# Performance work log

Measured on AMD Instinct MI355X. Metric: run time of the kernel, lower is better.

The kernel has to match this reference:

```python
import jax, jax.numpy as jnp
import numpy as np
import math

H = 512
N2 = 32  # N // 2
L_VAL = 8192
DT_MIN, DT_MAX = 0.001, 0.1


def setup_inputs() -> dict:
    key = jax.random.key(0)
    k1, k2, k3 = jax.random.split(key, 3)
    log_dt = jax.random.uniform(k1, (H,), dtype=jnp.float32) * (
        math.log(DT_MAX) - math.log(DT_MIN)) + math.log(DT_MIN)
    B_real = jax.random.normal(k2, (H, N2), dtype=jnp.float32)
    B_imag = jax.random.normal(k3, (H, N2), dtype=jnp.float32)
    C = jnp.ones((H, N2), dtype=jnp.float32)
    Kc = jnp.ones((H, N2), dtype=jnp.float32)
    A_real = jnp.log(0.5 * jnp.ones((H, N2), dtype=jnp.float32))
    A_imag = jnp.broadcast_to(math.pi * jnp.arange(N2, dtype=jnp.float32), (H, N2))
    return {"log_dt": log_dt, "B_real": B_real, "B_imag": B_imag,
            "C": C, "Kc": Kc, "A_real": A_real, "A_imag": A_imag, "L": L_VAL}


def reference(log_dt, B_real, B_imag, C, Kc, A_real, A_imag, L):
    dt = jnp.exp(log_dt)[:, None]                      # (H, 1)
    A = -jnp.exp(A_real) - 1e-6 + 1j * A_imag          # (H, N2) complex
    denom = 1.0 - dt * A / 2 + 1e-6                    # bilinear denominator
    dtA = (1.0 + dt * A / 2) / denom                   # discretized A (H, N2)
    B = B_real + 1j * B_imag
    dtB = dt * B / denom                               # discretized B (H, N2)
    log_dtA = jnp.log(dtA)                             # complex log
    # Vandermonde in log space: (H, N2, L) complex — the big intermediate.
    V = jnp.exp(log_dtA[:, :, None] * jnp.arange(L, dtype=jnp.float32))
    Cc = C.astype(dtB.dtype) * dtB                     # (H, N2) complex
    K = 2.0 * jnp.einsum('hn,hnl->hl', Cc, V).real     # (H, L)
    return K
```

## Files before the change

### kernel.cpp

```cpp
#include <hip/hip_runtime.h>
#include <math.h>

#define HN   512
#define N2M  32
#define LVAL 8192
#define TPB  256
#define STR  136
#define STRD 68

typedef _Float16 f16x8 __attribute__((ext_vector_type(8)));
typedef float    f32x4 __attribute__((ext_vector_type(4)));

__device__ __forceinline__ void split_store(unsigned* dst_hi, unsigned* dst_lo,
                                            float x, float y) {
    const _Float16 hx = (_Float16)x, hy = (_Float16)y;
    const float lxf = x - (float)hx, lyf = y - (float)hy;
    const _Float16 lx = (_Float16)lxf, ly = (_Float16)lyf;
    const unsigned short ux = __builtin_bit_cast(unsigned short, hx);
    const unsigned short uy = __builtin_bit_cast(unsigned short, hy);
    const unsigned short vx = __builtin_bit_cast(unsigned short, lx);
    const unsigned short vy = __builtin_bit_cast(unsigned short, ly);
    *dst_hi = (unsigned)ux | ((unsigned)uy << 16);
    *dst_lo = (unsigned)vx | ((unsigned)vy << 16);
}

__global__ __launch_bounds__(TPB, 4) void s4d_mfma(
    const float* __restrict__ log_dt,
    const float* __restrict__ B_real,
    const float* __restrict__ B_imag,
    const float* __restrict__ Cmat,
    const float* __restrict__ A_real,
    const float* __restrict__ A_imag,
    float* __restrict__ out)
{
    __shared__ __align__(16) _Float16 shU[64 * STR];
    __shared__ __align__(16) _Float16 shW[64 * STR];
    __shared__ float pm[N2M][12];

    const int h  = blockIdx.y;
    const int bx = blockIdx.x;
    const int t  = threadIdx.x;

    if (t < N2M) {
        const int idx = h * N2M + t;
        const float dt  = expf(log_dt[h]);
        const float Are = -expf(A_real[idx]) - 1e-6f;
        const float Aim = A_imag[idx];
        const float hdt = 0.5f * dt;
        const float dre  = 1.0f - hdt * Are + 1e-6f;
        const float dim_ = -hdt * Aim;
        const float nre = 1.0f + hdt * Are;
        const float nim = hdt * Aim;
        const float inv = 1.0f / (dre * dre + dim_ * dim_);
        const float zr = (nre * dre + nim * dim_) * inv;
        const float zi = (nim * dre - nre * dim_) * inv;
        const float br = B_real[idx], bi = B_imag[idx];
        const float tbr = dt * ((br * dre + bi * dim_) * inv);
        const float tbi = dt * ((bi * dre - br * dim_) * inv);
        const float Cv = Cmat[idx];
        const float c2r = 2.0f * Cv * tbr;
        const float c2i = 2.0f * Cv * tbi;
        const float r2  = zr * zr + zi * zi;
        const float xl2 = 0.5f * log2f(r2);
        const float phi = atan2f(zi, zr) * 0.15915494309189535f;
        const float ph  = __uint_as_float(__float_as_uint(phi) & 0xFFFFE000u);
        const float pl  = phi - ph;
        const float e64   = __builtin_amdgcn_exp2f(64.0f * xl2);
        const float rev64 = __builtin_amdgcn_fractf(
            fmaf(64.0f, pl, __builtin_amdgcn_fractf(64.0f * ph)));
        const float z64r = e64 * __builtin_amdgcn_cosf(rev64);
        const float z64i = e64 * __builtin_amdgcn_sinf(rev64);
        pm[t][0] = xl2; pm[t][1] = ph;  pm[t][2] = pl;
        pm[t][3] = c2r; pm[t][4] = c2i;
        pm[t][5] = zr;  pm[t][6] = zi;
        pm[t][7] = z64r; pm[t][8] = z64i;
    }
    __syncthreads();

    {
        const int n  = t >> 3;
        const int j0 = (t & 7) * 8;
        const float xl2 = pm[n][0], ph = pm[n][1], pl = pm[n][2];
        const float zr  = pm[n][5], zi = pm[n][6];
        const float j0f = (float)j0;
        const float e   = __builtin_amdgcn_exp2f(j0f * xl2);
        const float rev = __builtin_amdgcn_fractf(
            fmaf(j0f, pl, __builtin_amdgcn_fractf(j0f * ph)));
        float wr = e * __builtin_amdgcn_cosf(rev);
        float wi = e * __builtin_amdgcn_sinf(rev);
        unsigned* dw = (unsigned*)shW;
#pragma unroll
        for (int jj = 0; jj < 8; ++jj) {
            const int j = j0 + jj;
            split_store(dw + j * STRD + n, dw + j * STRD + 32 + n, wr, -wi);
            const float nwr = wr * zr - wi * zi;
            wi = fmaf(wr, zi, wi * zr);
            wr = nwr;
        }
    }

    {
        const int n  = t >> 3;
        const int m0 = (t & 7) * 8;
        const float xl2 = pm[n][0], ph = pm[n][1], pl = pm[n][2];
        const float c2r = pm[n][3], c2i = pm[n][4];
        const float z64r = pm[n][7], z64i = pm[n][8];
        const float l0f = (float)((bx << 12) + (m0 << 6));
        const float e   = __builtin_amdgcn_exp2f(l0f * xl2);
        const float rev = __builtin_amdgcn_fractf(
            fmaf(l0f, pl, __builtin_amdgcn_fractf(l0f * ph)));
        const float cs_ = __builtin_amdgcn_cosf(rev);
        const float sn_ = __builtin_amdgcn_sinf(rev);
        float ur = e * fmaf(c2r, cs_, -(c2i * sn_));
        float ui = e * fmaf(c2r, sn_, c2i * cs_);
        unsigned* dw = (unsigned*)shU;
#pragma unroll
        for (int mm = 0; mm < 8; ++mm) {
            const int m = m0 + mm;
            split_store(dw + m * STRD + n, dw + m * STRD + 32 + n, ur, ui);
            const float nur = ur * z64r - ui * z64i;
            ui = fmaf(ur, z64i, ui * z64r);
            ur = nur;
        }
    }
    __syncthreads();

    const int w = t >> 6, lane = t & 63, g = lane >> 4, r = lane & 15;
    const _Float16* ua = shU + (w * 16 + r) * STR + g * 8;
    const f16x8 A0 = *(const f16x8*)(ua);
    const f16x8 A1 = *(const f16x8*)(ua + 32);
    const f16x8 A2 = *(const f16x8*)(ua + 64);
    const f16x8 A3 = *(const f16x8*)(ua + 96);
    float* outp = out + (size_t)h * LVAL + (bx << 12);
#pragma unroll
    for (int jt = 0; jt < 4; ++jt) {
        const _Float16* wb = shW + (jt * 16 + r) * STR + g * 8;
        const f16x8 B0 = *(const f16x8*)(wb);
        const f16x8 B1 = *(const f16x8*)(wb + 32);
        const f16x8 B2 = *(const f16x8*)(wb + 64);
        const f16x8 B3 = *(const f16x8*)(wb + 96);
        f32x4 acc = {0.f, 0.f, 0.f, 0.f};
        acc = __builtin_amdgcn_mfma_f32_16x16x32_f16(A0, B0, acc, 0, 0, 0);
        acc = __builtin_amdgcn_mfma_f32_16x16x32_f16(A1, B1, acc, 0, 0, 0);
        acc = __builtin_amdgcn_mfma_f32_16x16x32_f16(A2, B0, acc, 0, 0, 0);
        acc = __builtin_amdgcn_mfma_f32_16x16x32_f16(A3, B1, acc, 0, 0, 0);
        acc = __builtin_amdgcn_mfma_f32_16x16x32_f16(A0, B2, acc, 0, 0, 0);
        acc = __builtin_amdgcn_mfma_f32_16x16x32_f16(A1, B3, acc, 0, 0, 0);
        const int jcol = jt * 16 + r;
#pragma unroll
        for (int rr = 0; rr < 4; ++rr) {
            const int m_local = w * 16 + g * 4 + rr;
            outp[m_local * 64 + jcol] = acc[rr];
        }
    }
}

extern "C" void kernel_launch(void* const* d_in, const int* in_sizes, int n_in,
                              void* d_out, int out_size, void* d_ws, size_t ws_size,
                              hipStream_t stream)
{
    const float* log_dt = (const float*)d_in[0];
    const float* B_real = (const float*)d_in[1];
    const float* B_imag = (const float*)d_in[2];
    const float* Cmat   = (const float*)d_in[3];
    const float* A_real = (const float*)d_in[5];
    const float* A_imag = (const float*)d_in[6];
    float* out = (float*)d_out;

    dim3 grid(2, HN);
    s4d_mfma<<<grid, dim3(TPB), 0, stream>>>(log_dt, B_real, B_imag, Cmat,
                                             A_real, A_imag, out);
}
```

Measured before the change: 13.58 us.

## Split per-mode parameter setup into a separate precompute kernel via workspace

Moves the per-(h,n) discretization math (exp, log2, atan2, sin/cos) out of the MFMA kernel into a small setup kernel that writes 12 floats per mode to the workspace. The main kernel then loads these with float4 reads into shared memory instead of having 32 threads compute them serially while the rest of the block waits. This removes the duplicated setup across the two x-blocks per row and shortens the serial prologue. In exchange it adds a second kernel launch and a global round trip, and drops the occupancy hint from launch_bounds.

```diff
diff --git a/kernel.cpp b/kernel.cpp
--- a/kernel.cpp
+++ b/kernel.cpp
@@ -24,64 +24,74 @@
     *dst_lo = (unsigned)vx | ((unsigned)vy << 16);
 }
 
-__global__ __launch_bounds__(TPB, 4) void s4d_mfma(
+__global__ __launch_bounds__(128) void s4d_setup(
     const float* __restrict__ log_dt,
     const float* __restrict__ B_real,
     const float* __restrict__ B_imag,
     const float* __restrict__ Cmat,
     const float* __restrict__ A_real,
     const float* __restrict__ A_imag,
+    float* __restrict__ ws)
+{
+    const int i = blockIdx.x * 128 + threadIdx.x;
+    if (i >= HN * N2M) return;
+    const int h = i >> 5;
+    const float dt  = expf(log_dt[h]);
+    const float Are = -expf(A_real[i]) - 1e-6f;
+    const float Aim = A_imag[i];
+    const float hdt = 0.5f * dt;
+    const float dre  = 1.0f - hdt * Are + 1e-6f;
+    const float dim_ = -hdt * Aim;
+    const float nre = 1.0f + hdt * Are;
+    const float nim = hdt * Aim;
+    const float inv = 1.0f / (dre * dre + dim_ * dim_);
+    const float zr = (nre * dre + nim * dim_) * inv;
+    const float zi = (nim * dre - nre * dim_) * inv;
+    const float br = B_real[i], bi = B_imag[i];
+    const float tbr = dt * ((br * dre + bi * dim_) * inv);
+    const float tbi = dt * ((bi * dre - br * dim_) * inv);
+    const float Cv = Cmat[i];
+    const float c2r = 2.0f * Cv * tbr;
+    const float c2i = 2.0f * Cv * tbi;
+    const float r2  = zr * zr + zi * zi;
+    const float xl2 = 0.5f * log2f(r2);
+    const float phi = atan2f(zi, zr) * 0.15915494309189535f;
+    const float ph  = __uint_as_float(__float_as_uint(phi) & 0xFFFFE000u);
+    const float pl  = phi - ph;
+    const float e64   = __builtin_amdgcn_exp2f(64.0f * xl2);
+    const float rev64 = __builtin_amdgcn_fractf(
+        fmaf(64.0f, pl, __builtin_amdgcn_fractf(64.0f * ph)));
+    const float z64r = e64 * __builtin_amdgcn_cosf(rev64);
+    const float z64i = e64 * __builtin_amdgcn_sinf(rev64);
+    float4* w4 = (float4*)(ws + (size_t)i * 12);
+    w4[0] = make_float4(xl2, ph, pl, c2r);
+    w4[1] = make_float4(c2i, zr, zi, z64r);
+    w4[2] = make_float4(z64i, 0.0f, 0.0f, 0.0f);
+}
+
+__global__ __launch_bounds__(TPB) void s4d_mfma(
+    const float* __restrict__ ws,
     float* __restrict__ out)
 {
     __shared__ __align__(16) _Float16 shU[64 * STR];
     __shared__ __align__(16) _Float16 shW[64 * STR];
-    __shared__ float pm[N2M][12];
+    __shared__ float4 pm4[N2M * 3];
 
     const int h  = blockIdx.y;
     const int bx = blockIdx.x;
     const int t  = threadIdx.x;
 
-    if (t < N2M) {
-        const int idx = h * N2M + t;
-        const float dt  = expf(log_dt[h]);
-        const float Are = -expf(A_real[idx]) - 1e-6f;
-        const float Aim = A_imag[idx];
-        const float hdt = 0.5f * dt;
-        const float dre  = 1.0f - hdt * Are + 1e-6f;
-        const float dim_ = -hdt * Aim;
-        const float nre = 1.0f + hdt * Are;
-        const float nim = hdt * Aim;
-        const float inv = 1.0f / (dre * dre + dim_ * dim_);
-        const float zr = (nre * dre + nim * dim_) * inv;
-        const float zi = (nim * dre - nre * dim_) * inv;
-        const float br = B_real[idx], bi = B_imag[idx];
-        const float tbr = dt * ((br * dre + bi * dim_) * inv);
-        const float tbi = dt * ((bi * dre - br * dim_) * inv);
-        const float Cv = Cmat[idx];
-        const float c2r = 2.0f * Cv * tbr;
-        const float c2i = 2.0f * Cv * tbi;
-        const float r2  = zr * zr + zi * zi;
-        const float xl2 = 0.5f * log2f(r2);
-        const float phi = atan2f(zi, zr) * 0.15915494309189535f;
-        const float ph  = __uint_as_float(__float_as_uint(phi) & 0xFFFFE000u);
-        const float pl  = phi - ph;
-        const float e64   = __builtin_amdgcn_exp2f(64.0f * xl2);
-        const float rev64 = __builtin_amdgcn_fractf(
-            fmaf(64.0f, pl, __builtin_amdgcn_fractf(64.0f * ph)));
-        const float z64r = e64 * __builtin_amdgcn_cosf(rev64);
-        const float z64i = e64 * __builtin_amdgcn_sinf(rev64);
-        pm[t][0] = xl2; pm[t][1] = ph;  pm[t][2] = pl;
-        pm[t][3] = c2r; pm[t][4] = c2i;
-        pm[t][5] = zr;  pm[t][6] = zi;
-        pm[t][7] = z64r; pm[t][8] = z64i;
+    if (t < N2M * 3) {
+        pm4[t] = ((const float4*)ws)[h * (N2M * 3) + t];
     }
     __syncthreads();
+    const float* pm = (const float*)pm4;
 
     {
         const int n  = t >> 3;
         const int j0 = (t & 7) * 8;
-        const float xl2 = pm[n][0], ph = pm[n][1], pl = pm[n][2];
-        const float zr  = pm[n][5], zi = pm[n][6];
+        const float xl2 = pm[n * 12 + 0], ph = pm[n * 12 + 1], pl = pm[n * 12 + 2];
+        const float zr  = pm[n * 12 + 5], zi = pm[n * 12 + 6];
         const float j0f = (float)j0;
         const float e   = __builtin_amdgcn_exp2f(j0f * xl2);
         const float rev = __builtin_amdgcn_fractf(
@@ -102,9 +112,9 @@
     {
         const int n  = t >> 3;
         const int m0 = (t & 7) * 8;
-        const float xl2 = pm[n][0], ph = pm[n][1], pl = pm[n][2];
-        const float c2r = pm[n][3], c2i = pm[n][4];
-        const float z64r = pm[n][7], z64i = pm[n][8];
+        const float xl2 = pm[n * 12 + 0], ph = pm[n * 12 + 1], pl = pm[n * 12 + 2];
+        const float c2r = pm[n * 12 + 3], c2i = pm[n * 12 + 4];
+        const float z64r = pm[n * 12 + 7], z64i = pm[n * 12 + 8];
         const float l0f = (float)((bx << 12) + (m0 << 6));
         const float e   = __builtin_amdgcn_exp2f(l0f * xl2);
         const float rev = __builtin_amdgcn_fractf(
@@ -166,8 +176,11 @@
     const float* A_real = (const float*)d_in[5];
     const float* A_imag = (const float*)d_in[6];
     float* out = (float*)d_out;
+    float* ws  = (float*)d_ws;
+
+    s4d_setup<<<dim3((HN * N2M) / 128), dim3(128), 0, stream>>>(
+        log_dt, B_real, B_imag, Cmat, A_real, A_imag, ws);
 
     dim3 grid(2, HN);
-    s4d_mfma<<<grid, dim3(TPB), 0, stream>>>(log_dt, B_real, B_imag, Cmat,
-                                             A_real, A_imag, out);
+    s4d_mfma<<<grid, dim3(TPB), 0, stream>>>(ws, out);
 }
```

Measured after the change: 18.00 us. 1.33x slower.

## Process one head per 512-thread block, swap MFMA operands for vector stores

Applied to the files above, without the earlier changes.

Each block now covers a full head (L=8192) with 512 threads instead of two blocks of 256. The W tile is generated once per head rather than once per half, and the shared U table grows to 128 rows. MFMA operand roles are swapped so each lane holds four consecutive output columns and writes them with one float4 store instead of four strided scalar stores. The hi/lo fp16 split now uses packed cvt_pkrtz conversions. The larger block adds LDS pressure and may lower occupancy, and round-toward-zero rounding slightly changes the hi/lo split.

```diff
diff --git a/kernel.cpp b/kernel.cpp
--- a/kernel.cpp
+++ b/kernel.cpp
@@ -4,24 +4,22 @@
 #define HN   512
 #define N2M  32
 #define LVAL 8192
-#define TPB  256
+#define TPB  512
 #define STR  136
 #define STRD 68
 
 typedef _Float16 f16x8 __attribute__((ext_vector_type(8)));
+typedef __fp16   pk16x2 __attribute__((ext_vector_type(2)));
 typedef float    f32x4 __attribute__((ext_vector_type(4)));
 
-__device__ __forceinline__ void split_store(unsigned* dst_hi, unsigned* dst_lo,
-                                            float x, float y) {
-    const _Float16 hx = (_Float16)x, hy = (_Float16)y;
-    const float lxf = x - (float)hx, lyf = y - (float)hy;
-    const _Float16 lx = (_Float16)lxf, ly = (_Float16)lyf;
-    const unsigned short ux = __builtin_bit_cast(unsigned short, hx);
-    const unsigned short uy = __builtin_bit_cast(unsigned short, hy);
-    const unsigned short vx = __builtin_bit_cast(unsigned short, lx);
-    const unsigned short vy = __builtin_bit_cast(unsigned short, ly);
-    *dst_hi = (unsigned)ux | ((unsigned)uy << 16);
-    *dst_lo = (unsigned)vx | ((unsigned)vy << 16);
+__device__ __forceinline__ void split_store_pk(unsigned* dhi, unsigned* dlo,
+                                               float x, float y) {
+    const pk16x2 hi = __builtin_amdgcn_cvt_pkrtz(x, y);
+    const float rx = x - (float)hi.x;
+    const float ry = y - (float)hi.y;
+    const pk16x2 lo = __builtin_amdgcn_cvt_pkrtz(rx, ry);
+    *dhi = __builtin_bit_cast(unsigned, hi);
+    *dlo = __builtin_bit_cast(unsigned, lo);
 }
 
 __global__ __launch_bounds__(TPB, 4) void s4d_mfma(
@@ -33,13 +31,12 @@
     const float* __restrict__ A_imag,
     float* __restrict__ out)
 {
-    __shared__ __align__(16) _Float16 shU[64 * STR];
+    __shared__ __align__(16) _Float16 shU[128 * STR];
     __shared__ __align__(16) _Float16 shW[64 * STR];
     __shared__ float pm[N2M][12];
 
-    const int h  = blockIdx.y;
-    const int bx = blockIdx.x;
-    const int t  = threadIdx.x;
+    const int h = blockIdx.x;
+    const int t = threadIdx.x;
 
     if (t < N2M) {
         const int idx = h * N2M + t;
@@ -65,80 +62,83 @@
         const float phi = atan2f(zi, zr) * 0.15915494309189535f;
         const float ph  = __uint_as_float(__float_as_uint(phi) & 0xFFFFE000u);
         const float pl  = phi - ph;
-        const float e64   = __builtin_amdgcn_exp2f(64.0f * xl2);
-        const float rev64 = __builtin_amdgcn_fractf(
-            fmaf(64.0f, pl, __builtin_amdgcn_fractf(64.0f * ph)));
-        const float z64r = e64 * __builtin_amdgcn_cosf(rev64);
-        const float z64i = e64 * __builtin_amdgcn_sinf(rev64);
+        const float e16   = __builtin_amdgcn_exp2f(16.0f * xl2);
+        const float rv16  = __builtin_amdgcn_fractf(
+            fmaf(16.0f, pl, __builtin_amdgcn_fractf(16.0f * ph)));
+        const float z16r = e16 * __builtin_amdgcn_cosf(rv16);
+        const float z16i = e16 * __builtin_amdgcn_sinf(rv16);
+        const float e1k   = __builtin_amdgcn_exp2f(1024.0f * xl2);
+        const float rv1k  = __builtin_amdgcn_fractf(
+            fmaf(1024.0f, pl, __builtin_amdgcn_fractf(1024.0f * ph)));
+        const float zkr = e1k * __builtin_amdgcn_cosf(rv1k);
+        const float zki = e1k * __builtin_amdgcn_sinf(rv1k);
         pm[t][0] = xl2; pm[t][1] = ph;  pm[t][2] = pl;
         pm[t][3] = c2r; pm[t][4] = c2i;
-        pm[t][5] = zr;  pm[t][6] = zi;
-        pm[t][7] = z64r; pm[t][8] = z64i;
+        pm[t][5] = z16r; pm[t][6] = z16i;
+        pm[t][7] = zkr;  pm[t][8] = zki;
     }
     __syncthreads();
 
+    const int n  = t >> 4;
+    const int lg = t & 15;
+    const float xl2 = pm[n][0], ph = pm[n][1], pl = pm[n][2];
+
     {
-        const int n  = t >> 3;
-        const int j0 = (t & 7) * 8;
-        const float xl2 = pm[n][0], ph = pm[n][1], pl = pm[n][2];
-        const float zr  = pm[n][5], zi = pm[n][6];
-        const float j0f = (float)j0;
-        const float e   = __builtin_amdgcn_exp2f(j0f * xl2);
+        const float jf  = (float)lg;
+        const float e   = __builtin_amdgcn_exp2f(jf * xl2);
         const float rev = __builtin_amdgcn_fractf(
-            fmaf(j0f, pl, __builtin_amdgcn_fractf(j0f * ph)));
+            fmaf(jf, pl, __builtin_amdgcn_fractf(jf * ph)));
         float wr = e * __builtin_amdgcn_cosf(rev);
         float wi = e * __builtin_amdgcn_sinf(rev);
+        const float sr = pm[n][5], si = pm[n][6];
         unsigned* dw = (unsigned*)shW;
 #pragma unroll
-        for (int jj = 0; jj < 8; ++jj) {
-            const int j = j0 + jj;
-            split_store(dw + j * STRD + n, dw + j * STRD + 32 + n, wr, -wi);
-            const float nwr = wr * zr - wi * zi;
-            wi = fmaf(wr, zi, wi * zr);
-            wr = nwr;
+        for (int s = 0; s < 4; ++s) {
+            const int j = lg + 16 * s;
+            split_store_pk(dw + j * STRD + n, dw + j * STRD + 32 + n, wr, -wi);
+            const float nr = wr * sr - wi * si;
+            wi = fmaf(wr, si, wi * sr);
+            wr = nr;
         }
     }
 
     {
-        const int n  = t >> 3;
-        const int m0 = (t & 7) * 8;
-        const float xl2 = pm[n][0], ph = pm[n][1], pl = pm[n][2];
-        const float c2r = pm[n][3], c2i = pm[n][4];
-        const float z64r = pm[n][7], z64i = pm[n][8];
-        const float l0f = (float)((bx << 12) + (m0 << 6));
+        const float l0f = (float)(lg << 6);
         const float e   = __builtin_amdgcn_exp2f(l0f * xl2);
         const float rev = __builtin_amdgcn_fractf(
             fmaf(l0f, pl, __builtin_amdgcn_fractf(l0f * ph)));
         const float cs_ = __builtin_amdgcn_cosf(rev);
         const float sn_ = __builtin_amdgcn_sinf(rev);
+        const float c2r = pm[n][3], c2i = pm[n][4];
         float ur = e * fmaf(c2r, cs_, -(c2i * sn_));
         float ui = e * fmaf(c2r, sn_, c2i * cs_);
-        unsigned* dw = (unsigned*)shU;
+        const float sr = pm[n][7], si = pm[n][8];
+        unsigned* du = (unsigned*)shU;
 #pragma unroll
-        for (int mm = 0; mm < 8; ++mm) {
-            const int m = m0 + mm;
-            split_store(dw + m * STRD + n, dw + m * STRD + 32 + n, ur, ui);
-            const float nur = ur * z64r - ui * z64i;
-            ui = fmaf(ur, z64i, ui * z64r);
-            ur = nur;
+        for (int s = 0; s < 8; ++s) {
+            const int m = lg + 16 * s;
+            split_store_pk(du + m * STRD + n, du + m * STRD + 32 + n, ur, ui);
+            const float nr = ur * sr - ui * si;
+            ui = fmaf(ur, si, ui * sr);
+            ur = nr;
         }
     }
     __syncthreads();
 
     const int w = t >> 6, lane = t & 63, g = lane >> 4, r = lane & 15;
-    const _Float16* ua = shU + (w * 16 + r) * STR + g * 8;
-    const f16x8 A0 = *(const f16x8*)(ua);
-    const f16x8 A1 = *(const f16x8*)(ua + 32);
-    const f16x8 A2 = *(const f16x8*)(ua + 64);
-    const f16x8 A3 = *(const f16x8*)(ua + 96);
-    float* outp = out + (size_t)h * LVAL + (bx << 12);
+    const _Float16* ub = shU + (w * 16 + r) * STR + g * 8;
+    const f16x8 B0 = *(const f16x8*)(ub);
+    const f16x8 B1 = *(const f16x8*)(ub + 32);
+    const f16x8 B2 = *(const f16x8*)(ub + 64);
+    const f16x8 B3 = *(const f16x8*)(ub + 96);
+    float* outp = out + (size_t)h * LVAL;
 #pragma unroll
     for (int jt = 0; jt < 4; ++jt) {
-        const _Float16* wb = shW + (jt * 16 + r) * STR + g * 8;
-        const f16x8 B0 = *(const f16x8*)(wb);
-        const f16x8 B1 = *(const f16x8*)(wb + 32);
-        const f16x8 B2 = *(const f16x8*)(wb + 64);
-        const f16x8 B3 = *(const f16x8*)(wb + 96);
+        const _Float16* wa = shW + (jt * 16 + r) * STR + g * 8;
+        const f16x8 A0 = *(const f16x8*)(wa);
+        const f16x8 A1 = *(const f16x8*)(wa + 32);
+        const f16x8 A2 = *(const f16x8*)(wa + 64);
+        const f16x8 A3 = *(const f16x8*)(wa + 96);
         f32x4 acc = {0.f, 0.f, 0.f, 0.f};
         acc = __builtin_amdgcn_mfma_f32_16x16x32_f16(A0, B0, acc, 0, 0, 0);
         acc = __builtin_amdgcn_mfma_f32_16x16x32_f16(A1, B1, acc, 0, 0, 0);
@@ -146,12 +146,8 @@
         acc = __builtin_amdgcn_mfma_f32_16x16x32_f16(A3, B1, acc, 0, 0, 0);
         acc = __builtin_amdgcn_mfma_f32_16x16x32_f16(A0, B2, acc, 0, 0, 0);
         acc = __builtin_amdgcn_mfma_f32_16x16x32_f16(A1, B3, acc, 0, 0, 0);
-        const int jcol = jt * 16 + r;
-#pragma unroll
-        for (int rr = 0; rr < 4; ++rr) {
-            const int m_local = w * 16 + g * 4 + rr;
-            outp[m_local * 64 + jcol] = acc[rr];
-        }
+        float4 v = make_float4(acc[0], acc[1], acc[2], acc[3]);
+        *(float4*)(outp + 64 * (16 * w + r) + 16 * jt + 4 * g) = v;
     }
 }
 
@@ -167,7 +163,6 @@
     const float* A_imag = (const float*)d_in[6];
     float* out = (float*)d_out;
 
-    dim3 grid(2, HN);
-    s4d_mfma<<<grid, dim3(TPB), 0, stream>>>(log_dt, B_real, B_imag, Cmat,
-                                             A_real, A_imag, out);
+    s4d_mfma<<<dim3(HN), dim3(TPB), 0, stream>>>(log_dt, B_real, B_imag, Cmat,
+                                                 A_real, A_imag, out);
 }
```

Measured after the change: 12.00 us. -11.6%, faster.
